# Kernel optimization log

Measured on AMD Instinct MI355X. Metric: run time of the kernel, lower is better.

Reference implementation:

```python
import jax, jax.numpy as jnp
import numpy as np

EPS = 1e-06

def setup_inputs() -> dict:
    key = jax.random.key(0)
    k1, k2, k3 = jax.random.split(key, 3)
    N, L, H, D = 4, 4096, 16, 64
    return {
        "queries": jax.random.normal(k1, (N, L, H, D), dtype=jnp.float32),
        "keys": jax.random.normal(k2, (N, L, H, D), dtype=jnp.float32),
        "values": jax.random.normal(k3, (N, L, H, D), dtype=jnp.float32),
    }

def reference(queries, keys, values):
    # [N, L, H, D] -> [N, H, L, D]
    q = jnp.transpose(queries, (0, 2, 1, 3))
    k = jnp.transpose(keys, (0, 2, 1, 3))
    v = jnp.transpose(values, (0, 2, 1, 3))
    # kernel feature map
    q = jax.nn.sigmoid(q)
    k = jax.nn.sigmoid(k)
    L = q.shape[2]
    S = k.shape[2]
    # incoming/outgoing flow normalizers
    normalizer_row = 1.0 / jnp.einsum('nhld,nhd->nhl', q + EPS, k.sum(axis=2) + EPS)
    normalizer_col = 1.0 / jnp.einsum('nhsd,nhd->nhs', k + EPS, q.sum(axis=2) + EPS)
    # refined normalizers (competition / allocation)
    row_refine = jnp.einsum('nhld,nhd->nhl', q + EPS,
                            (k * normalizer_col[..., None]).sum(axis=2) + EPS)
    col_refine = jnp.einsum('nhsd,nhd->nhs', k + EPS,
                            (q * normalizer_row[..., None]).sum(axis=2) + EPS)
    row_refine = jax.nn.sigmoid(row_refine * (float(L) / float(S)))
    col_refine = jax.nn.softmax(col_refine, axis=-1) * S
    # linear attention aggregation: kv is [N, H, D, D]
    kv = jnp.einsum('nhsd,nhse->nhde', k, v * col_refine[..., None])
    x = jnp.einsum('nhld,nhde->nhle', q, kv) * (normalizer_row * row_refine)[..., None]
    # back to [N, L, H, D]
    return jnp.transpose(x, (0, 2, 1, 3))
```

## Files before the change

### kernel.cpp

```cpp
#include <hip/hip_runtime.h>
#include <math.h>

#define EPS 1e-6f
constexpr int N_ = 4, L_ = 4096, H_ = 16, D_ = 64;
constexpr int NH = N_ * H_;
constexpr int HD = H_ * D_;
constexpr long NSTRIDE = (long)L_ * HD;
constexpr int SCHUNKS = 16;
constexpr int KSB = 2048;

typedef __attribute__((ext_vector_type(8))) short short8;
typedef __attribute__((ext_vector_type(4))) float f32x4;

__device__ float g_qsum[NH * D_];
__device__ float g_ksum[NH * D_];
__device__ float g_qnr[NH * D_];
__device__ float g_knc[NH * D_];
__device__ float g_kv[NH * D_ * D_];
__device__ float g_kvpart[(long)SCHUNKS * NH * D_ * D_];
__device__ float g_kncpart[SCHUNKS * NH * D_];
__device__ float g_ssumpart[SCHUNKS * NH];
__device__ float g_partK[(long)KSB * 1024];
__device__ float g_partQs[(long)KSB * 1024];
__device__ float g_partQn[(long)KSB * 1024];

__device__ __forceinline__ float sigm(float x) {
    return 1.0f / (1.0f + __expf(-x));
}
__device__ __forceinline__ float4 sigm4(float4 x) {
    float4 r;
    r.x = sigm(x.x); r.y = sigm(x.y); r.z = sigm(x.z); r.w = sigm(x.w);
    return r;
}
__device__ __forceinline__ float red16(float p) {
    p += __shfl_xor(p, 1);
    p += __shfl_xor(p, 2);
    p += __shfl_xor(p, 4);
    p += __shfl_xor(p, 8);
    return p;
}
__device__ __forceinline__ unsigned rne_hi(unsigned xb) {
    return (xb + 0x7fffu + ((xb >> 16) & 1u)) & 0xffff0000u;
}
__device__ __forceinline__ uint2 split2(float x) {
    unsigned h1 = rne_hi(__float_as_uint(x));
    float r = x - __uint_as_float(h1);
    unsigned h2 = rne_hi(__float_as_uint(r));
    return make_uint2(h1, h2);
}
union U8 { unsigned u[4]; short8 s; };

__global__ __launch_bounds__(256, 8) void kA_ksum(const float* __restrict__ k) {
    int t = threadIdx.x;
    long g0 = (long)blockIdx.x * 8;
    const float* p = k + g0 * HD + t * 4;
    float4 x[8];
#pragma unroll
    for (int r = 0; r < 8; ++r) x[r] = *(const float4*)(p + (long)r * HD);
    float ax = 0.f, ay = 0.f, az = 0.f, aw = 0.f;
#pragma unroll
    for (int r = 0; r < 8; ++r) {
        float4 s = sigm4(x[r]);
        ax += s.x; ay += s.y; az += s.z; aw += s.w;
    }
    float4 o = {ax, ay, az, aw};
    *(float4*)&g_partK[((long)blockIdx.x << 10) + t * 4] = o;
}

__global__ __launch_bounds__(256, 8) void kB_q(const float* __restrict__ q) {
    int t = threadIdx.x;
    long g0 = (long)blockIdx.x * 8;
    int n = (int)(g0 >> 12);
    float4 bv = *(const float4*)(g_ksum + n * 1024 + t * 4);
    bv.x += EPS; bv.y += EPS; bv.z += EPS; bv.w += EPS;
    const float* p = q + g0 * HD + t * 4;
    float4 x[8];
#pragma unroll
    for (int r = 0; r < 8; ++r) x[r] = *(const float4*)(p + (long)r * HD);
    float sx = 0.f, sy = 0.f, sz = 0.f, sw = 0.f;
    float nx = 0.f, ny = 0.f, nz = 0.f, nw = 0.f;
#pragma unroll
    for (int r = 0; r < 8; ++r) {
        float4 s = sigm4(x[r]);
        sx += s.x; sy += s.y; sz += s.z; sw += s.w;
        float pd = (s.x + EPS) * bv.x + (s.y + EPS) * bv.y
                 + (s.z + EPS) * bv.z + (s.w + EPS) * bv.w;
        pd = red16(pd);
        float inv = 1.0f / pd;
        nx += s.x * inv; ny += s.y * inv; nz += s.z * inv; nw += s.w * inv;
    }
    float4 os = {sx, sy, sz, sw};
    float4 on = {nx, ny, nz, nw};
    *(float4*)&g_partQs[((long)blockIdx.x << 10) + t * 4] = os;
    *(float4*)&g_partQn[((long)blockIdx.x << 10) + t * 4] = on;
}

__global__ __launch_bounds__(256) void kred(int mode) {
    int t = threadIdx.x, z = blockIdx.y;
    const float* src = (mode == 0) ? g_partK : (z ? g_partQn : g_partQs);
    float* dst = (mode == 0) ? g_ksum : (z ? g_qnr : g_qsum);
    int n = blockIdx.x & 3, cc = blockIdx.x >> 2;
    int c = cc * 128 + (t & 31) * 4;
    int bg = t >> 5;
    float sx = 0.f, sy = 0.f, sz = 0.f, sw = 0.f;
#pragma unroll 4
    for (int i = 0; i < 64; ++i) {
        long b = n * 512 + bg * 64 + i;
        float4 p = *(const float4*)&src[(b << 10) + c];
        sx += p.x; sy += p.y; sz += p.z; sw += p.w;
    }
    __shared__ float4 esb[256];
    esb[t] = make_float4(sx, sy, sz, sw);
    __syncthreads();
    if (t < 32) {
        float4 s = esb[t];
#pragma unroll
        for (int g = 1; g < 8; ++g) {
            float4 b2 = esb[t + g * 32];
            s.x += b2.x; s.y += b2.y; s.z += b2.z; s.w += b2.w;
        }
        *(float4*)&dst[n * 1024 + cc * 128 + t * 4] = s;
    }
}

__global__ __launch_bounds__(256, 4) void k4_kv(const float* __restrict__ k,
                                                const float* __restrict__ v) {
    int nh = blockIdx.y, n = nh >> 4, h = nh & 15;
    int t = threadIdx.x, lane = t & 63, wv = t >> 6;
    __shared__ unsigned kA[16 * 66], kB[16 * 66], vA[16 * 66], vB[16 * 66];
    __shared__ float kncred[16 * 64];
    __shared__ float esb[256];
    int sp = t >> 4, c4 = t & 15;
    long nbase = (long)n * NSTRIDE + (long)h * D_;
    int s0blk = blockIdx.x * 256;
    float4 qn = *(const float4*)&g_qnr[nh * 64 + c4 * 4];
    qn.x += EPS; qn.y += EPS; qn.z += EPS; qn.w += EPS;
    float4 qs = *(const float4*)&g_qsum[nh * 64 + c4 * 4];
    qs.x += EPS; qs.y += EPS; qs.z += EPS; qs.w += EPS;

    f32x4 acc[4];
#pragma unroll
    for (int e = 0; e < 4; ++e) acc[e] = (f32x4){0.f, 0.f, 0.f, 0.f};
    int m = lane & 15, qd = lane >> 4;
    float esum = 0.f;
    float knx = 0.f, kny = 0.f, knz = 0.f, knw = 0.f;

    float4 ke, ko, ve, vo;
    {
        long gb = nbase + (long)(s0blk + 2 * sp) * HD + c4 * 4;
        ke = *(const float4*)&k[gb]; ko = *(const float4*)&k[gb + HD];
        ve = *(const float4*)&v[gb]; vo = *(const float4*)&v[gb + HD];
    }
    for (int st = 0; st < 8; ++st) {
        float4 se = sigm4(ke), so = sigm4(ko);
        float pde = (se.x + EPS) * qn.x + (se.y + EPS) * qn.y
                  + (se.z + EPS) * qn.z + (se.w + EPS) * qn.w;
        float pdo = (so.x + EPS) * qn.x + (so.y + EPS) * qn.y
                  + (so.z + EPS) * qn.z + (so.w + EPS) * qn.w;
        float pne = (se.x + EPS) * qs.x + (se.y + EPS) * qs.y
                  + (se.z + EPS) * qs.z + (se.w + EPS) * qs.w;
        float pno = (so.x + EPS) * qs.x + (so.y + EPS) * qs.y
                  + (so.z + EPS) * qs.z + (so.w + EPS) * qs.w;
        pde = red16(pde); pdo = red16(pdo);
        pne = red16(pne); pno = red16(pno);
        float ee = __expf(pde), eo = __expf(pdo);
        if (c4 == 0) esum += ee + eo;
        float nce = 1.0f / pne, nco = 1.0f / pno;
        knx += se.x * nce + so.x * nco;
        kny += se.y * nce + so.y * nco;
        knz += se.z * nce + so.z * nco;
        knw += se.w * nce + so.w * nco;
        se.x *= ee; se.y *= ee; se.z *= ee; se.w *= ee;
        so.x *= eo; so.y *= eo; so.z *= eo; so.w *= eo;
        uint2 a0 = split2(se.x), a1_ = split2(se.y), a2_ = split2(se.z), a3_ = split2(se.w);
        uint2 b0 = split2(so.x), b1_ = split2(so.y), b2_ = split2(so.z), b3_ = split2(so.w);
        unsigned kaw0 = (a0.x >> 16) | (b0.x & 0xffff0000u);
        unsigned kaw1 = (a1_.x >> 16) | (b1_.x & 0xffff0000u);
        unsigned kaw2 = (a2_.x >> 16) | (b2_.x & 0xffff0000u);
        unsigned kaw3 = (a3_.x >> 16) | (b3_.x & 0xffff0000u);
        unsigned kbw0 = (a0.y >> 16) | (b0.y & 0xffff0000u);
        unsigned kbw1 = (a1_.y >> 16) | (b1_.y & 0xffff0000u);
        unsigned kbw2 = (a2_.y >> 16) | (b2_.y & 0xffff0000u);
        unsigned kbw3 = (a3_.y >> 16) | (b3_.y & 0xffff0000u);
        uint2 c0 = split2(ve.x), c1 = split2(ve.y), c2 = split2(ve.z), c3 = split2(ve.w);
        uint2 d0 = split2(vo.x), d1 = split2(vo.y), d2 = split2(vo.z), d3 = split2(vo.w);
        unsigned vaw0 = (c0.x >> 16) | (d0.x & 0xffff0000u);
        unsigned vaw1 = (c1.x >> 16) | (d1.x & 0xffff0000u);
        unsigned vaw2 = (c2.x >> 16) | (d2.x & 0xffff0000u);
        unsigned vaw3 = (c3.x >> 16) | (d3.x & 0xffff0000u);
        unsigned vbw0 = (c0.y >> 16) | (d0.y & 0xffff0000u);
        unsigned vbw1 = (c1.y >> 16) | (d1.y & 0xffff0000u);
        unsigned vbw2 = (c2.y >> 16) | (d2.y & 0xffff0000u);
        unsigned vbw3 = (c3.y >> 16) | (d3.y & 0xffff0000u);
        __syncthreads();
        int wb = sp * 66 + c4 * 4;
        *(uint2*)&kA[wb] = make_uint2(kaw0, kaw1); *(uint2*)&kA[wb + 2] = make_uint2(kaw2, kaw3);
        *(uint2*)&kB[wb] = make_uint2(kbw0, kbw1); *(uint2*)&kB[wb + 2] = make_uint2(kbw2, kbw3);
        *(uint2*)&vA[wb] = make_uint2(vaw0, vaw1); *(uint2*)&vA[wb + 2] = make_uint2(vaw2, vaw3);
        *(uint2*)&vB[wb] = make_uint2(vbw0, vbw1); *(uint2*)&vB[wb + 2] = make_uint2(vbw2, vbw3);
        __syncthreads();
        if (st < 7) {
            long gb = nbase + (long)(s0blk + (st + 1) * 32 + 2 * sp) * HD + c4 * 4;
            ke = *(const float4*)&k[gb]; ko = *(const float4*)&k[gb + HD];
            ve = *(const float4*)&v[gb]; vo = *(const float4*)&v[gb + HD];
        }
        U8 fa1, fa2;
#pragma unroll
        for (int jp = 0; jp < 4; ++jp) {
            int idx = (qd * 4 + jp) * 66 + wv * 16 + m;
            fa1.u[jp] = kA[idx]; fa2.u[jp] = kB[idx];
        }
#pragma unroll
        for (int e = 0; e < 4; ++e) {
            U8 fb1, fb2;
#pragma unroll
            for (int jp = 0; jp < 4; ++jp) {
                int idx = (qd * 4 + jp) * 66 + e * 16 + m;
                fb1.u[jp] = vA[idx]; fb2.u[jp] = vB[idx];
            }
            acc[e] = __builtin_amdgcn_mfma_f32_16x16x32_bf16(fa1.s, fb2.s, acc[e], 0, 0, 0);
            acc[e] = __builtin_amdgcn_mfma_f32_16x16x32_bf16(fa2.s, fb1.s, acc[e], 0, 0, 0);
            acc[e] = __builtin_amdgcn_mfma_f32_16x16x32_bf16(fa1.s, fb1.s, acc[e], 0, 0, 0);
        }
    }
    float* dst = &g_kvpart[((long)blockIdx.x * NH + nh) * 4096];
#pragma unroll
    for (int e = 0; e < 4; ++e)
#pragma unroll
        for (int r = 0; r < 4; ++r)
            dst[(wv * 16 + qd * 4 + r) * 64 + e * 16 + m] = acc[e][r];
    *(float4*)&kncred[sp * 64 + c4 * 4] = make_float4(knx, kny, knz, knw);
    esb[t] = esum;
    __syncthreads();
    if (t < 64) {
        float s = 0.f;
#pragma unroll
        for (int i = 0; i < 16; ++i) s += kncred[i * 64 + t];
        g_kncpart[(blockIdx.x * NH + nh) * 64 + t] = s;
    }
    for (int s2 = 128; s2; s2 >>= 1) {
        if (t < s2) esb[t] += esb[t + s2];
        __syncthreads();
    }
    if (t == 0) g_ssumpart[blockIdx.x * NH + nh] = esb[0];
}

__global__ __launch_bounds__(256) void k4b_reduce() {
    int nh = blockIdx.x, t = threadIdx.x;
    float ssum = 0.f;
#pragma unroll
    for (int c = 0; c < SCHUNKS; ++c) ssum += g_ssumpart[c * NH + nh];
    float scale = (float)L_ / ssum;
    int i4 = blockIdx.y * 256 + t;
    float sx = 0.f, sy = 0.f, sz = 0.f, sw = 0.f;
#pragma unroll
    for (int c = 0; c < SCHUNKS; ++c) {
        float4 p = *(const float4*)&g_kvpart[((long)c * NH + nh) * 4096 + i4 * 4];
        sx += p.x; sy += p.y; sz += p.z; sw += p.w;
    }
    float4 o = {sx * scale, sy * scale, sz * scale, sw * scale};
    *(float4*)&g_kv[nh * 4096 + i4 * 4] = o;
    if (blockIdx.y == 0 && t < 64) {
        float s = 0.f;
#pragma unroll
        for (int c = 0; c < SCHUNKS; ++c) s += g_kncpart[(c * NH + nh) * 64 + t];
        g_knc[nh * 64 + t] = s;
    }
}

__global__ __launch_bounds__(256, 4) void k5_out(const float* __restrict__ q,
                                                 float* __restrict__ out) {
    int nh = blockIdx.y, n = nh >> 4, h = nh & 15;
    int t = threadIdx.x, lane = t & 63, wv = t >> 6;
    __shared__ unsigned qA[32 * 66], qB[32 * 66], kvA[32 * 66], kvB[32 * 66];
    __shared__ float coef[64];
    int c4 = t & 15;
    long nbase = (long)n * NSTRIDE + (long)h * D_;
    int l0 = blockIdx.x * 64;
    float4 bk1 = *(const float4*)&g_ksum[nh * 64 + c4 * 4];
    float4 bk2 = *(const float4*)&g_knc[nh * 64 + c4 * 4];
    bk1.x += EPS; bk1.y += EPS; bk1.z += EPS; bk1.w += EPS;
    bk2.x += EPS; bk2.y += EPS; bk2.z += EPS; bk2.w += EPS;
    float4 xe[2], xo[2];
#pragma unroll
    for (int j = 0; j < 2; ++j) {
        int slot = t + j * 256;
        int dp = slot >> 4, cc = slot & 15;
        const float* kvr = &g_kv[nh * 4096 + (2 * dp) * 64 + cc * 4];
        xe[j] = *(const float4*)kvr;
        xo[j] = *(const float4*)(kvr + 64);
    }
    float4 xq[4];
#pragma unroll
    for (int j = 0; j < 4; ++j) {
        int r = (t >> 4) + j * 16;
        xq[j] = *(const float4*)&q[nbase + (long)(l0 + r) * HD + c4 * 4];
    }
#pragma unroll
    for (int j = 0; j < 2; ++j) {
        int slot = t + j * 256;
        int dp = slot >> 4, cc = slot & 15;
        uint2 e0 = split2(xe[j].x), e1 = split2(xe[j].y), e2 = split2(xe[j].z), e3 = split2(xe[j].w);
        uint2 o0 = split2(xo[j].x), o1 = split2(xo[j].y), o2 = split2(xo[j].z), o3 = split2(xo[j].w);
        int wb = dp * 66 + cc * 4;
        *(uint2*)&kvA[wb] = make_uint2((e0.x >> 16) | (o0.x & 0xffff0000u),
                                       (e1.x >> 16) | (o1.x & 0xffff0000u));
        *(uint2*)&kvA[wb + 2] = make_uint2((e2.x >> 16) | (o2.x & 0xffff0000u),
                                           (e3.x >> 16) | (o3.x & 0xffff0000u));
        *(uint2*)&kvB[wb] = make_uint2((e0.y >> 16) | (o0.y & 0xffff0000u),
                                       (e1.y >> 16) | (o1.y & 0xffff0000u));
        *(uint2*)&kvB[wb + 2] = make_uint2((e2.y >> 16) | (o2.y & 0xffff0000u),
                                           (e3.y >> 16) | (o3.y & 0xffff0000u));
    }
#pragma unroll
    for (int j = 0; j < 4; ++j) {
        int r = (t >> 4) + j * 16;
        float4 s = sigm4(xq[j]);
        float p1 = (s.x + EPS) * bk1.x + (s.y + EPS) * bk1.y
                 + (s.z + EPS) * bk1.z + (s.w + EPS) * bk1.w;
        float p2 = (s.x + EPS) * bk2.x + (s.y + EPS) * bk2.y
                 + (s.z + EPS) * bk2.z + (s.w + EPS) * bk2.w;
        p1 = red16(p1); p2 = red16(p2);
        if (c4 == 0) coef[r] = sigm(p2) / p1;
        uint2 t0 = split2(s.x), t1 = split2(s.y), t2 = split2(s.z), t3 = split2(s.w);
        qA[(c4 * 2) * 66 + r]     = (t0.x >> 16) | (t1.x & 0xffff0000u);
        qB[(c4 * 2) * 66 + r]     = (t0.y >> 16) | (t1.y & 0xffff0000u);
        qA[(c4 * 2 + 1) * 66 + r] = (t2.x >> 16) | (t3.x & 0xffff0000u);
        qB[(c4 * 2 + 1) * 66 + r] = (t2.y >> 16) | (t3.y & 0xffff0000u);
    }
    __syncthreads();
    int m = lane & 15, qd = lane >> 4;
    f32x4 acc[4];
#pragma unroll
    for (int e = 0; e < 4; ++e) acc[e] = (f32x4){0.f, 0.f, 0.f, 0.f};
#pragma unroll
    for (int kk = 0; kk < 2; ++kk) {
        U8 fa1, fa2;
#pragma unroll
        for (int jp = 0; jp < 4; ++jp) {
            int idx = (kk * 16 + qd * 4 + jp) * 66 + wv * 16 + m;
            fa1.u[jp] = qA[idx]; fa2.u[jp] = qB[idx];
        }
#pragma unroll
        for (int e = 0; e < 4; ++e) {
            U8 fb1, fb2;
#pragma unroll
            for (int jp = 0; jp < 4; ++jp) {
                int idx = (kk * 16 + qd * 4 + jp) * 66 + e * 16 + m;
                fb1.u[jp] = kvA[idx]; fb2.u[jp] = kvB[idx];
            }
            acc[e] = __builtin_amdgcn_mfma_f32_16x16x32_bf16(fa1.s, fb2.s, acc[e], 0, 0, 0);
            acc[e] = __builtin_amdgcn_mfma_f32_16x16x32_bf16(fa2.s, fb1.s, acc[e], 0, 0, 0);
            acc[e] = __builtin_amdgcn_mfma_f32_16x16x32_bf16(fa1.s, fb1.s, acc[e], 0, 0, 0);
        }
    }
#pragma unroll
    for (int e = 0; e < 4; ++e)
#pragma unroll
        for (int r = 0; r < 4; ++r) {
            int ll = wv * 16 + qd * 4 + r;
            out[nbase + (long)(l0 + ll) * HD + e * 16 + m] = acc[e][r] * coef[ll];
        }
}

extern "C" void kernel_launch(void* const* d_in, const int* in_sizes, int n_in,
                              void* d_out, int out_size, void* d_ws, size_t ws_size,
                              hipStream_t stream) {
    const float* q = (const float*)d_in[0];
    const float* k = (const float*)d_in[1];
    const float* v = (const float*)d_in[2];
    float* out = (float*)d_out;

    kA_ksum<<<KSB, 256, 0, stream>>>(k);
    kred<<<dim3(32, 1), 256, 0, stream>>>(0);
    kB_q<<<KSB, 256, 0, stream>>>(q);
    kred<<<dim3(32, 2), 256, 0, stream>>>(1);
    k4_kv<<<dim3(SCHUNKS, NH), 256, 0, stream>>>(k, v);
    k4b_reduce<<<dim3(NH, 4), 256, 0, stream>>>();
    k5_out<<<dim3(L_ / 64, NH), 256, 0, stream>>>(q, out);
}
```

Baseline: 281.0 us.

## Replace partial-sum reduction kernels with atomics, DPP reductions, double-buffered LDS

The two partial-sum reduction kernels and their large scratch buffers are dropped. The column sums are now accumulated with global float atomicAdd from each block, after a small zeroing kernel. The 16-lane shuffle reductions use DPP row operations instead of ds_swizzle/bpermute shuffles. The k/v MFMA loop gains double-buffered LDS planes and an earlier prefetch, which removes one barrier per step. The cost is atomic contention (512 blocks per output address) and a summation order that is no longer deterministic.

```diff
diff --git a/kernel.cpp b/kernel.cpp
--- a/kernel.cpp
+++ b/kernel.cpp
@@ -7,7 +7,6 @@
 constexpr int HD = H_ * D_;
 constexpr long NSTRIDE = (long)L_ * HD;
 constexpr int SCHUNKS = 16;
-constexpr int KSB = 2048;
 
 typedef __attribute__((ext_vector_type(8))) short short8;
 typedef __attribute__((ext_vector_type(4))) float f32x4;
@@ -20,9 +19,6 @@
 __device__ float g_kvpart[(long)SCHUNKS * NH * D_ * D_];
 __device__ float g_kncpart[SCHUNKS * NH * D_];
 __device__ float g_ssumpart[SCHUNKS * NH];
-__device__ float g_partK[(long)KSB * 1024];
-__device__ float g_partQs[(long)KSB * 1024];
-__device__ float g_partQn[(long)KSB * 1024];
 
 __device__ __forceinline__ float sigm(float x) {
     return 1.0f / (1.0f + __expf(-x));
@@ -32,11 +28,16 @@
     r.x = sigm(x.x); r.y = sigm(x.y); r.z = sigm(x.z); r.w = sigm(x.w);
     return r;
 }
+template <int CTRL>
+__device__ __forceinline__ float dpp_add(float x) {
+    int y = __builtin_amdgcn_update_dpp(0, __float_as_int(x), CTRL, 0xf, 0xf, true);
+    return x + __int_as_float(y);
+}
 __device__ __forceinline__ float red16(float p) {
-    p += __shfl_xor(p, 1);
-    p += __shfl_xor(p, 2);
-    p += __shfl_xor(p, 4);
-    p += __shfl_xor(p, 8);
+    p = dpp_add<0xB1>(p);
+    p = dpp_add<0x4E>(p);
+    p = dpp_add<0x141>(p);
+    p = dpp_add<0x140>(p);
     return p;
 }
 __device__ __forceinline__ unsigned rne_hi(unsigned xb) {
@@ -50,9 +51,18 @@
 }
 union U8 { unsigned u[4]; short8 s; };
 
+__global__ void k0_zero() {
+    int i = blockIdx.x * 256 + threadIdx.x;
+    float4 z = {0.f, 0.f, 0.f, 0.f};
+    if (i < 1024) *(float4*)&g_ksum[i * 4] = z;
+    else if (i < 2048) *(float4*)&g_qsum[(i - 1024) * 4] = z;
+    else if (i < 3072) *(float4*)&g_qnr[(i - 2048) * 4] = z;
+}
+
 __global__ __launch_bounds__(256, 8) void kA_ksum(const float* __restrict__ k) {
     int t = threadIdx.x;
     long g0 = (long)blockIdx.x * 8;
+    int n = (int)(g0 >> 12);
     const float* p = k + g0 * HD + t * 4;
     float4 x[8];
 #pragma unroll
@@ -63,8 +73,11 @@
         float4 s = sigm4(x[r]);
         ax += s.x; ay += s.y; az += s.z; aw += s.w;
     }
-    float4 o = {ax, ay, az, aw};
-    *(float4*)&g_partK[((long)blockIdx.x << 10) + t * 4] = o;
+    float* d0 = g_ksum + n * 1024 + t * 4;
+    atomicAdd(d0 + 0, ax);
+    atomicAdd(d0 + 1, ay);
+    atomicAdd(d0 + 2, az);
+    atomicAdd(d0 + 3, aw);
 }
 
 __global__ __launch_bounds__(256, 8) void kB_q(const float* __restrict__ q) {
@@ -89,45 +102,19 @@
         float inv = 1.0f / pd;
         nx += s.x * inv; ny += s.y * inv; nz += s.z * inv; nw += s.w * inv;
     }
-    float4 os = {sx, sy, sz, sw};
-    float4 on = {nx, ny, nz, nw};
-    *(float4*)&g_partQs[((long)blockIdx.x << 10) + t * 4] = os;
-    *(float4*)&g_partQn[((long)blockIdx.x << 10) + t * 4] = on;
-}
-
-__global__ __launch_bounds__(256) void kred(int mode) {
-    int t = threadIdx.x, z = blockIdx.y;
-    const float* src = (mode == 0) ? g_partK : (z ? g_partQn : g_partQs);
-    float* dst = (mode == 0) ? g_ksum : (z ? g_qnr : g_qsum);
-    int n = blockIdx.x & 3, cc = blockIdx.x >> 2;
-    int c = cc * 128 + (t & 31) * 4;
-    int bg = t >> 5;
-    float sx = 0.f, sy = 0.f, sz = 0.f, sw = 0.f;
-#pragma unroll 4
-    for (int i = 0; i < 64; ++i) {
-        long b = n * 512 + bg * 64 + i;
-        float4 p = *(const float4*)&src[(b << 10) + c];
-        sx += p.x; sy += p.y; sz += p.z; sw += p.w;
-    }
-    __shared__ float4 esb[256];
-    esb[t] = make_float4(sx, sy, sz, sw);
-    __syncthreads();
-    if (t < 32) {
-        float4 s = esb[t];
-#pragma unroll
-        for (int g = 1; g < 8; ++g) {
-            float4 b2 = esb[t + g * 32];
-            s.x += b2.x; s.y += b2.y; s.z += b2.z; s.w += b2.w;
-        }
-        *(float4*)&dst[n * 1024 + cc * 128 + t * 4] = s;
-    }
+    float* ds = g_qsum + n * 1024 + t * 4;
+    float* dn = g_qnr + n * 1024 + t * 4;
+    atomicAdd(ds + 0, sx); atomicAdd(ds + 1, sy);
+    atomicAdd(ds + 2, sz); atomicAdd(ds + 3, sw);
+    atomicAdd(dn + 0, nx); atomicAdd(dn + 1, ny);
+    atomicAdd(dn + 2, nz); atomicAdd(dn + 3, nw);
 }
 
 __global__ __launch_bounds__(256, 4) void k4_kv(const float* __restrict__ k,
                                                 const float* __restrict__ v) {
     int nh = blockIdx.y, n = nh >> 4, h = nh & 15;
     int t = threadIdx.x, lane = t & 63, wv = t >> 6;
-    __shared__ unsigned kA[16 * 66], kB[16 * 66], vA[16 * 66], vB[16 * 66];
+    __shared__ unsigned planes[2][4][16 * 66];
     __shared__ float kncred[16 * 64];
     __shared__ float esb[256];
     int sp = t >> 4, c4 = t & 15;
@@ -152,6 +139,12 @@
         ve = *(const float4*)&v[gb]; vo = *(const float4*)&v[gb + HD];
     }
     for (int st = 0; st < 8; ++st) {
+        float4 nke, nko, nve, nvo;
+        if (st < 7) {
+            long gb = nbase + (long)(s0blk + (st + 1) * 32 + 2 * sp) * HD + c4 * 4;
+            nke = *(const float4*)&k[gb]; nko = *(const float4*)&k[gb + HD];
+            nve = *(const float4*)&v[gb]; nvo = *(const float4*)&v[gb + HD];
+        }
         float4 se = sigm4(ke), so = sigm4(ko);
         float pde = (se.x + EPS) * qn.x + (se.y + EPS) * qn.y
                   + (se.z + EPS) * qn.z + (se.w + EPS) * qn.w;
@@ -174,41 +167,35 @@
         so.x *= eo; so.y *= eo; so.z *= eo; so.w *= eo;
         uint2 a0 = split2(se.x), a1_ = split2(se.y), a2_ = split2(se.z), a3_ = split2(se.w);
         uint2 b0 = split2(so.x), b1_ = split2(so.y), b2_ = split2(so.z), b3_ = split2(so.w);
-        unsigned kaw0 = (a0.x >> 16) | (b0.x & 0xffff0000u);
-        unsigned kaw1 = (a1_.x >> 16) | (b1_.x & 0xffff0000u);
-        unsigned kaw2 = (a2_.x >> 16) | (b2_.x & 0xffff0000u);
-        unsigned kaw3 = (a3_.x >> 16) | (b3_.x & 0xffff0000u);
-        unsigned kbw0 = (a0.y >> 16) | (b0.y & 0xffff0000u);
-        unsigned kbw1 = (a1_.y >> 16) | (b1_.y & 0xffff0000u);
-        unsigned kbw2 = (a2_.y >> 16) | (b2_.y & 0xffff0000u);
-        unsigned kbw3 = (a3_.y >> 16) | (b3_.y & 0xffff0000u);
         uint2 c0 = split2(ve.x), c1 = split2(ve.y), c2 = split2(ve.z), c3 = split2(ve.w);
         uint2 d0 = split2(vo.x), d1 = split2(vo.y), d2 = split2(vo.z), d3 = split2(vo.w);
-        unsigned vaw0 = (c0.x >> 16) | (d0.x & 0xffff0000u);
-        unsigned vaw1 = (c1.x >> 16) | (d1.x & 0xffff0000u);
-        unsigned vaw2 = (c2.x >> 16) | (d2.x & 0xffff0000u);
-        unsigned vaw3 = (c3.x >> 16) | (d3.x & 0xffff0000u);
-        unsigned vbw0 = (c0.y >> 16) | (d0.y & 0xffff0000u);
-        unsigned vbw1 = (c1.y >> 16) | (d1.y & 0xffff0000u);
-        unsigned vbw2 = (c2.y >> 16) | (d2.y & 0xffff0000u);
-        unsigned vbw3 = (c3.y >> 16) | (d3.y & 0xffff0000u);
+        unsigned* kAp = planes[st & 1][0];
+        unsigned* kBp = planes[st & 1][1];
+        unsigned* vAp = planes[st & 1][2];
+        unsigned* vBp = planes[st & 1][3];
+        int wb = sp * 66 + c4 * 4;
+        *(uint2*)&kAp[wb] = make_uint2((a0.x >> 16) | (b0.x & 0xffff0000u),
+                                       (a1_.x >> 16) | (b1_.x & 0xffff0000u));
+        *(uint2*)&kAp[wb + 2] = make_uint2((a2_.x >> 16) | (b2_.x & 0xffff0000u),
+                                           (a3_.x >> 16) | (b3_.x & 0xffff0000u));
+        *(uint2*)&kBp[wb] = make_uint2((a0.y >> 16) | (b0.y & 0xffff0000u),
+                                       (a1_.y >> 16) | (b1_.y & 0xffff0000u));
+        *(uint2*)&kBp[wb + 2] = make_uint2((a2_.y >> 16) | (b2_.y & 0xffff0000u),
+                                           (a3_.y >> 16) | (b3_.y & 0xffff0000u));
+        *(uint2*)&vAp[wb] = make_uint2((c0.x >> 16) | (d0.x & 0xffff0000u),
+                                       (c1.x >> 16) | (d1.x & 0xffff0000u));
+        *(uint2*)&vAp[wb + 2] = make_uint2((c2.x >> 16) | (d2.x & 0xffff0000u),
+                                           (c3.x >> 16) | (d3.x & 0xffff0000u));
+        *(uint2*)&vBp[wb] = make_uint2((c0.y >> 16) | (d0.y & 0xffff0000u),
+                                       (c1.y >> 16) | (d1.y & 0xffff0000u));
+        *(uint2*)&vBp[wb + 2] = make_uint2((c2.y >> 16) | (d2.y & 0xffff0000u),
+                                           (c3.y >> 16) | (d3.y & 0xffff0000u));
         __syncthreads();
-        int wb = sp * 66 + c4 * 4;
-        *(uint2*)&kA[wb] = make_uint2(kaw0, kaw1); *(uint2*)&kA[wb + 2] = make_uint2(kaw2, kaw3);
-        *(uint2*)&kB[wb] = make_uint2(kbw0, kbw1); *(uint2*)&kB[wb + 2] = make_uint2(kbw2, kbw3);
-        *(uint2*)&vA[wb] = make_uint2(vaw0, vaw1); *(uint2*)&vA[wb + 2] = make_uint2(vaw2, vaw3);
-        *(uint2*)&vB[wb] = make_uint2(vbw0, vbw1); *(uint2*)&vB[wb + 2] = make_uint2(vbw2, vbw3);
-        __syncthreads();
-        if (st < 7) {
-            long gb = nbase + (long)(s0blk + (st + 1) * 32 + 2 * sp) * HD + c4 * 4;
-            ke = *(const float4*)&k[gb]; ko = *(const float4*)&k[gb + HD];
-            ve = *(const float4*)&v[gb]; vo = *(const float4*)&v[gb + HD];
-        }
         U8 fa1, fa2;
 #pragma unroll
         for (int jp = 0; jp < 4; ++jp) {
             int idx = (qd * 4 + jp) * 66 + wv * 16 + m;
-            fa1.u[jp] = kA[idx]; fa2.u[jp] = kB[idx];
+            fa1.u[jp] = kAp[idx]; fa2.u[jp] = kBp[idx];
         }
 #pragma unroll
         for (int e = 0; e < 4; ++e) {
@@ -216,12 +203,13 @@
 #pragma unroll
             for (int jp = 0; jp < 4; ++jp) {
                 int idx = (qd * 4 + jp) * 66 + e * 16 + m;
-                fb1.u[jp] = vA[idx]; fb2.u[jp] = vB[idx];
+                fb1.u[jp] = vAp[idx]; fb2.u[jp] = vBp[idx];
             }
             acc[e] = __builtin_amdgcn_mfma_f32_16x16x32_bf16(fa1.s, fb2.s, acc[e], 0, 0, 0);
             acc[e] = __builtin_amdgcn_mfma_f32_16x16x32_bf16(fa2.s, fb1.s, acc[e], 0, 0, 0);
             acc[e] = __builtin_amdgcn_mfma_f32_16x16x32_bf16(fa1.s, fb1.s, acc[e], 0, 0, 0);
         }
+        if (st < 7) { ke = nke; ko = nko; ve = nve; vo = nvo; }
     }
     float* dst = &g_kvpart[((long)blockIdx.x * NH + nh) * 4096];
 #pragma unroll
@@ -371,10 +359,9 @@
     const float* v = (const float*)d_in[2];
     float* out = (float*)d_out;
 
-    kA_ksum<<<KSB, 256, 0, stream>>>(k);
-    kred<<<dim3(32, 1), 256, 0, stream>>>(0);
-    kB_q<<<KSB, 256, 0, stream>>>(q);
-    kred<<<dim3(32, 2), 256, 0, stream>>>(1);
+    k0_zero<<<12, 256, 0, stream>>>();
+    kA_ksum<<<2048, 256, 0, stream>>>(k);
+    kB_q<<<2048, 256, 0, stream>>>(q);
     k4_kv<<<dim3(SCHUNKS, NH), 256, 0, stream>>>(k, v);
     k4b_reduce<<<dim3(NH, 4), 256, 0, stream>>>();
     k5_out<<<dim3(L_ / 64, NH), 256, 0, stream>>>(q, out);
```

Measured after the change: 624.1 us. 2.22x slower.
